# Optimization experiments

Measured on AMD Instinct MI355X. Metric: run time of the kernel, lower is better.

The kernel has to match this reference:

```python
import jax, jax.numpy as jnp
import numpy as np

N_NODES = 50000
DEG = 16
N_EDGES = N_NODES * DEG
IN_FEATS = 256
NUM_HEADS = 4
OUT_FEATS = 64
NEG_SLOPE = 0.2


def setup_inputs() -> dict:
    key = jax.random.key(0)
    k1, k2, k3, k4, k5, k6 = jax.random.split(key, 6)
    row_ptr = jnp.arange(N_NODES + 1, dtype=jnp.int64 if jax.config.jax_enable_x64 else jnp.int32) * DEG
    col_ind = jax.random.randint(k1, (N_EDGES,), 0, N_NODES)
    # CSC mirrors (used only by the fused op's backward pass; math-inert here)
    col_ptr = jnp.arange(N_NODES + 1, dtype=row_ptr.dtype) * DEG
    row_ind = jax.random.randint(k2, (N_EDGES,), 0, N_NODES)
    feat = jax.random.normal(k3, (N_NODES, IN_FEATS), dtype=jnp.float32)
    # Glorot-style init for params
    g = float(np.sqrt(2.0))  # gain for relu
    std_W = g * np.sqrt(2.0 / (IN_FEATS + OUT_FEATS * NUM_HEADS))
    W = jax.random.normal(k4, (IN_FEATS, OUT_FEATS * NUM_HEADS), dtype=jnp.float32) * std_W
    std_a = g * np.sqrt(2.0 / (1 + NUM_HEADS * OUT_FEATS))
    attn_l = jax.random.normal(k5, (1, NUM_HEADS, OUT_FEATS), dtype=jnp.float32) * std_a
    attn_r = jax.random.normal(k6, (1, NUM_HEADS, OUT_FEATS), dtype=jnp.float32) * std_a
    return {"row_ptr": row_ptr, "col_ind": col_ind, "col_ptr": col_ptr,
            "row_ind": row_ind, "feat": feat, "W": W, "attn_l": attn_l, "attn_r": attn_r}


def reference(row_ptr, col_ind, col_ptr, row_ind, feat, W, attn_l, attn_r):
    N = feat.shape[0]
    E = col_ind.shape[0]
    # Dense projection: [N, H, F]
    h = jnp.matmul(feat, W).reshape(N, NUM_HEADS, OUT_FEATS)
    attn_row = jnp.sum(attn_l * h, axis=-1)  # [N, H] (dst scores)
    attn_col = jnp.sum(attn_r * h, axis=-1)  # [N, H] (src scores)
    # Recover destination node id per edge from CSR row_ptr
    dst = jnp.searchsorted(row_ptr, jnp.arange(E), side="right") - 1  # [E]
    src = col_ind  # [E]
    # Edge score: LeakyReLU(attn_row[dst] + attn_col[src])
    e = attn_row[dst] + attn_col[src]  # [E, H]
    e = jnp.where(e > 0, e, NEG_SLOPE * e)
    # Segment softmax over each destination's neighborhood
    e_max = jax.ops.segment_max(e, dst, num_segments=N)  # [N, H]
    ex = jnp.exp(e - e_max[dst])  # [E, H]
    denom = jax.ops.segment_sum(ex, dst, num_segments=N)  # [N, H]
    alpha = ex / denom[dst]  # [E, H]
    # Weighted scatter-add aggregation of source features
    out = jax.ops.segment_sum(h[src] * alpha[:, :, None], dst, num_segments=N)  # [N, H, F]
    return out
```

## Files before the change

kernel.cpp:

```cpp
#include <hip/hip_runtime.h>
#include <hip/hip_bf16.h>

#define DEG        16
#define IN_FEATS   256
#define NUM_HEADS  4
#define OUT_FEATS  64
#define HF         256
#define NEG_SLOPE  0.2f

#define CPITCH 264

typedef __attribute__((ext_vector_type(8))) short  short8;
typedef __attribute__((ext_vector_type(4))) float  floatx4;
typedef unsigned short ushortT;

__device__ __forceinline__ unsigned short f2bf(float f) {
    union { float f; unsigned u; } v; v.f = f;
    unsigned r = v.u + 0x7fffu + ((v.u >> 16) & 1u);
    return (unsigned short)(r >> 16);
}
__device__ __forceinline__ float bf_lo(unsigned u) {
    union { unsigned x; float f; } v; v.x = u << 16; return v.f;
}
__device__ __forceinline__ float bf_hi(unsigned u) {
    union { unsigned x; float f; } v; v.x = u & 0xffff0000u; return v.f;
}
__device__ __forceinline__ unsigned cvt2(float lo, float hi) {
    return (unsigned)f2bf(lo) | ((unsigned)f2bf(hi) << 16);
}

__global__ __launch_bounds__(256) void conv_wt(
    const float* __restrict__ W, ushortT* __restrict__ Wt)
{
    int n = blockIdx.x;
    int k = threadIdx.x;
    Wt[n * 256 + k] = f2bf(W[k * 256 + n]);
}

__global__ __launch_bounds__(256) void gat_gemm_fused(
    const float* __restrict__ feat,
    const ushortT* __restrict__ Bt,
    const float* __restrict__ attn_l,
    const float* __restrict__ attn_r,
    ushortT* __restrict__ Hb,
    float* __restrict__ arow,
    float* __restrict__ acol,
    int M)
{
    __shared__ __align__(16) ushortT SMEM[32 * CPITCH];
    ushortT* As = SMEM;
    ushortT* Cs = SMEM;

    const int tid  = threadIdx.x;
    const int wave = tid >> 6;
    const int lane = tid & 63;
    const int l15  = lane & 15;
    const int quad = lane >> 4;
    const int rowBase = blockIdx.x * 32;

    short8 bbuf[2][4];
    #pragma unroll
    for (int ni = 0; ni < 4; ++ni)
        bbuf[0][ni] = *(const short8*)&Bt[(wave * 64 + ni * 16 + l15) * 256 + quad * 8];

    {
        float4 v[8];
        #pragma unroll
        for (int i = 0; i < 8; ++i) {
            int id  = i * 256 + tid;
            int row = id >> 6;
            int c4  = id & 63;
            int gr  = rowBase + row; if (gr > M - 1) gr = M - 1;
            v[i] = *(const float4*)&feat[(size_t)gr * 256 + c4 * 4];
        }
        #pragma unroll
        for (int i = 0; i < 8; ++i) {
            int id   = i * 256 + tid;
            int row  = id >> 6;
            int c4   = id & 63;
            int cg   = c4 >> 1;
            int half = c4 & 1;
            uint2 w = make_uint2(cvt2(v[i].x, v[i].y), cvt2(v[i].z, v[i].w));
            *(uint2*)&As[row * 256 + ((cg ^ (row & 7)) << 3) + half * 4] = w;
        }
    }

    __syncthreads();

    floatx4 acc[2][4] = {};

    #pragma unroll
    for (int ks = 0; ks < 8; ++ks) {
        if (ks < 7) {
            #pragma unroll
            for (int ni = 0; ni < 4; ++ni)
                bbuf[(ks + 1) & 1][ni] = *(const short8*)
                    &Bt[(wave * 64 + ni * 16 + l15) * 256 + (ks + 1) * 32 + quad * 8];
        }
        short8 af[2];
        #pragma unroll
        for (int mi = 0; mi < 2; ++mi) {
            int row = mi * 16 + l15;
            int q   = ks * 4 + quad;
            int cst = q ^ (row & 7);
            af[mi] = *(const short8*)&As[row * 256 + cst * 8];
        }
        #pragma unroll
        for (int mi = 0; mi < 2; ++mi)
            #pragma unroll
            for (int ni = 0; ni < 4; ++ni)
                acc[mi][ni] = __builtin_amdgcn_mfma_f32_16x16x32_bf16(
                    af[mi], bbuf[ks & 1][ni], acc[mi][ni], 0, 0, 0);
    }

    float al[4], ar[4];
    #pragma unroll
    for (int ni = 0; ni < 4; ++ni) {
        al[ni] = attn_l[wave * 64 + ni * 16 + l15];
        ar[ni] = attn_r[wave * 64 + ni * 16 + l15];
    }
    #pragma unroll
    for (int mi = 0; mi < 2; ++mi) {
        #pragma unroll
        for (int reg = 0; reg < 4; ++reg) {
            float pl = 0.f, pr = 0.f;
            #pragma unroll
            for (int ni = 0; ni < 4; ++ni) {
                pl = fmaf(acc[mi][ni][reg], al[ni], pl);
                pr = fmaf(acc[mi][ni][reg], ar[ni], pr);
            }
            #pragma unroll
            for (int off = 8; off >= 1; off >>= 1) {
                pl += __shfl_xor(pl, off, 64);
                pr += __shfl_xor(pr, off, 64);
            }
            if (l15 == 0) {
                int gr = rowBase + mi * 16 + quad * 4 + reg;
                if (gr < M) {
                    arow[gr * NUM_HEADS + wave] = pl;
                    acol[gr * NUM_HEADS + wave] = pr;
                }
            }
        }
    }

    __syncthreads();

    #pragma unroll
    for (int mi = 0; mi < 2; ++mi)
        #pragma unroll
        for (int ni = 0; ni < 4; ++ni)
            #pragma unroll
            for (int reg = 0; reg < 4; ++reg)
                Cs[(mi * 16 + quad * 4 + reg) * CPITCH + wave * 64 + ni * 16 + l15] =
                    f2bf(acc[mi][ni][reg]);
    __syncthreads();

    #pragma unroll
    for (int i = 0; i < 4; ++i) {
        int f  = tid + 256 * i;
        int r  = f >> 5;
        int c8 = (f & 31) << 3;
        int gr = rowBase + r;
        if (gr < M) {
            uint4 v = *(const uint4*)&Cs[r * CPITCH + c8];
            *(uint4*)&Hb[(size_t)gr * HF + c8] = v;
        }
    }
}

__global__ __launch_bounds__(256) void gat_aggregate9(
    const ushortT* __restrict__ Hb,
    const float* __restrict__ arow,
    const float* __restrict__ acol,
    const int* __restrict__ col_ind,
    float* __restrict__ out,
    int N)
{
    const int tid  = threadIdx.x;
    const int wave = tid >> 6;
    const int lane = tid & 63;
    const int gw   = blockIdx.x * 4 + wave;

    int nA = gw * 2;
    if (nA >= N) return;
    int nB = nA + 1;
    const bool hasB = (nB < N);
    if (!hasB) nB = nA;

    const int j16  = lane & 15;
    const int hd16 = lane >> 4;

    int srcA = col_ind[nA * DEG + j16];
    int srcB = col_ind[nB * DEG + j16];
    float eA = arow[nA * NUM_HEADS + hd16] + acol[srcA * NUM_HEADS + hd16];
    float eB = arow[nB * NUM_HEADS + hd16] + acol[srcB * NUM_HEADS + hd16];
    eA = (eA > 0.f) ? eA : NEG_SLOPE * eA;
    eB = (eB > 0.f) ? eB : NEG_SLOPE * eB;

    float mA = eA, mB = eB;
    #pragma unroll
    for (int off = 8; off >= 1; off >>= 1) {
        mA = fmaxf(mA, __shfl_xor(mA, off, 16));
        mB = fmaxf(mB, __shfl_xor(mB, off, 16));
    }
    float exA = __expf(eA - mA), exB = __expf(eB - mB);
    float sA = exA, sB = exB;
    #pragma unroll
    for (int off = 8; off >= 1; off >>= 1) {
        sA += __shfl_xor(sA, off, 16);
        sB += __shfl_xor(sB, off, 16);
    }
    float alA = exA / sA;
    float alB = exB / sB;

    const int l32     = lane & 31;
    const int half    = lane >> 5;
    const int headSel = (l32 >> 3) << 4;

    int   sjA[8], sjB[8];
    float avA[8], avB[8];
    #pragma unroll
    for (int j = 0; j < 8; ++j) {
        int ep = (j << 1) + half;
        sjA[j] = __shfl(srcA, ep, 64);
        avA[j] = __shfl(alA, headSel + ep, 64);
        sjB[j] = __shfl(srcB, ep, 64);
        avB[j] = __shfl(alB, headSel + ep, 64);
    }

    uint4 vA[8], vB[8];
    #pragma unroll
    for (int j = 0; j < 8; ++j)
        vA[j] = *(const uint4*)&Hb[(size_t)sjA[j] * HF + l32 * 8];
    #pragma unroll
    for (int j = 0; j < 8; ++j)
        vB[j] = *(const uint4*)&Hb[(size_t)sjB[j] * HF + l32 * 8];

    __builtin_amdgcn_sched_barrier(0);

    float accA[8] = {}, accB[8] = {};
    #pragma unroll
    for (int j = 0; j < 8; ++j) {
        accA[0] = fmaf(avA[j], bf_lo(vA[j].x), accA[0]);
        accA[1] = fmaf(avA[j], bf_hi(vA[j].x), accA[1]);
        accA[2] = fmaf(avA[j], bf_lo(vA[j].y), accA[2]);
        accA[3] = fmaf(avA[j], bf_hi(vA[j].y), accA[3]);
        accA[4] = fmaf(avA[j], bf_lo(vA[j].z), accA[4]);
        accA[5] = fmaf(avA[j], bf_hi(vA[j].z), accA[5]);
        accA[6] = fmaf(avA[j], bf_lo(vA[j].w), accA[6]);
        accA[7] = fmaf(avA[j], bf_hi(vA[j].w), accA[7]);
    }
    #pragma unroll
    for (int j = 0; j < 8; ++j) {
        accB[0] = fmaf(avB[j], bf_lo(vB[j].x), accB[0]);
        accB[1] = fmaf(avB[j], bf_hi(vB[j].x), accB[1]);
        accB[2] = fmaf(avB[j], bf_lo(vB[j].y), accB[2]);
        accB[3] = fmaf(avB[j], bf_hi(vB[j].y), accB[3]);
        accB[4] = fmaf(avB[j], bf_lo(vB[j].z), accB[4]);
        accB[5] = fmaf(avB[j], bf_hi(vB[j].z), accB[5]);
        accB[6] = fmaf(avB[j], bf_lo(vB[j].w), accB[6]);
        accB[7] = fmaf(avB[j], bf_hi(vB[j].w), accB[7]);
    }

    #pragma unroll
    for (int i = 0; i < 8; ++i) {
        accA[i] += __shfl_xor(accA[i], 32, 64);
        accB[i] += __shfl_xor(accB[i], 32, 64);
    }

    float4 oA, oB;
    if (half == 0) {
        oA = make_float4(accA[0], accA[1], accA[2], accA[3]);
        oB = make_float4(accB[0], accB[1], accB[2], accB[3]);
    } else {
        oA = make_float4(accA[4], accA[5], accA[6], accA[7]);
        oB = make_float4(accB[4], accB[5], accB[6], accB[7]);
    }
    *(float4*)&out[(size_t)nA * HF + l32 * 8 + half * 4] = oA;
    if (hasB)
        *(float4*)&out[(size_t)nB * HF + l32 * 8 + half * 4] = oB;
}

extern "C" void kernel_launch(void* const* d_in, const int* in_sizes, int n_in,
                              void* d_out, int out_size, void* d_ws, size_t ws_size,
                              hipStream_t stream) {
    const int*   col_ind = (const int*)  d_in[1];
    const float* feat    = (const float*)d_in[4];
    const float* W       = (const float*)d_in[5];
    const float* attn_l  = (const float*)d_in[6];
    const float* attn_r  = (const float*)d_in[7];
    float* out = (float*)d_out;

    const int N = in_sizes[0] - 1;

    ushortT* Hb   = (ushortT*)d_ws;
    float*   arow = (float*)(Hb + (size_t)N * HF);
    float*   acol = arow + (size_t)N * NUM_HEADS;
    ushortT* Wt   = (ushortT*)(acol + (size_t)N * NUM_HEADS);

    conv_wt<<<256, 256, 0, stream>>>(W, Wt);

    dim3 ggrid((N + 31) / 32);
    gat_gemm_fused<<<ggrid, 256, 0, stream>>>(feat, Wt, attn_l, attn_r,
                                              Hb, arow, acol, N);

    gat_aggregate9<<<(N + 7) / 8, 256, 0, stream>>>(Hb, arow, acol, col_ind, out, N);
}
```

Baseline: 195.6 us.

## Make GEMM kernel persistent with register-resident W and prefetched feature tiles

Converts the projection GEMM into a persistent kernel with 512 blocks that loop over 32-row tiles. Each wave loads its whole bf16 W slice into registers once instead of streaming it per tile. The next tile's feature rows are prefetched into registers while the current tile runs its MFMAs. This cuts repeated W traffic and per-block launch and setup cost, but the 32 short8 register arrays raise VGPR pressure, which may lower occupancy or cause spills.

```diff
diff --git a/kernel.cpp b/kernel.cpp
--- a/kernel.cpp
+++ b/kernel.cpp
@@ -45,7 +45,7 @@
     ushortT* __restrict__ Hb,
     float* __restrict__ arow,
     float* __restrict__ acol,
-    int M)
+    int M, int nTiles)
 {
     __shared__ __align__(16) ushortT SMEM[32 * CPITCH];
     ushortT* As = SMEM;
@@ -56,23 +56,38 @@
     const int lane = tid & 63;
     const int l15  = lane & 15;
     const int quad = lane >> 4;
-    const int rowBase = blockIdx.x * 32;
-
-    short8 bbuf[2][4];
-    #pragma unroll
-    for (int ni = 0; ni < 4; ++ni)
-        bbuf[0][ni] = *(const short8*)&Bt[(wave * 64 + ni * 16 + l15) * 256 + quad * 8];
-
-    {
-        float4 v[8];
+
+    short8 Breg[8][4];
+    #pragma unroll
+    for (int ks = 0; ks < 8; ++ks)
+        #pragma unroll
+        for (int ni = 0; ni < 4; ++ni)
+            Breg[ks][ni] = *(const short8*)
+                &Bt[(wave * 64 + ni * 16 + l15) * 256 + ks * 32 + quad * 8];
+
+    float al[4], ar[4];
+    #pragma unroll
+    for (int ni = 0; ni < 4; ++ni) {
+        al[ni] = attn_l[wave * 64 + ni * 16 + l15];
+        ar[ni] = attn_r[wave * 64 + ni * 16 + l15];
+    }
+
+    int t = blockIdx.x;
+    float4 v[8];
+    if (t < nTiles) {
         #pragma unroll
         for (int i = 0; i < 8; ++i) {
             int id  = i * 256 + tid;
             int row = id >> 6;
             int c4  = id & 63;
-            int gr  = rowBase + row; if (gr > M - 1) gr = M - 1;
+            int gr  = t * 32 + row; if (gr > M - 1) gr = M - 1;
             v[i] = *(const float4*)&feat[(size_t)gr * 256 + c4 * 4];
         }
+    }
+
+    for (; t < nTiles; t += gridDim.x) {
+        const int rowBase = t * 32;
+
         #pragma unroll
         for (int i = 0; i < 8; ++i) {
             int id   = i * 256 + tid;
@@ -83,89 +98,90 @@
             uint2 w = make_uint2(cvt2(v[i].x, v[i].y), cvt2(v[i].z, v[i].w));
             *(uint2*)&As[row * 256 + ((cg ^ (row & 7)) << 3) + half * 4] = w;
         }
-    }
-
-    __syncthreads();
-
-    floatx4 acc[2][4] = {};
-
-    #pragma unroll
-    for (int ks = 0; ks < 8; ++ks) {
-        if (ks < 7) {
+        __syncthreads();
+
+        {
+            int t2 = t + gridDim.x;
+            if (t2 < nTiles) {
+                #pragma unroll
+                for (int i = 0; i < 8; ++i) {
+                    int id  = i * 256 + tid;
+                    int row = id >> 6;
+                    int c4  = id & 63;
+                    int gr  = t2 * 32 + row; if (gr > M - 1) gr = M - 1;
+                    v[i] = *(const float4*)&feat[(size_t)gr * 256 + c4 * 4];
+                }
+            }
+        }
+
+        floatx4 acc[2][4] = {};
+        #pragma unroll
+        for (int ks = 0; ks < 8; ++ks) {
+            short8 af[2];
             #pragma unroll
-            for (int ni = 0; ni < 4; ++ni)
-                bbuf[(ks + 1) & 1][ni] = *(const short8*)
-                    &Bt[(wave * 64 + ni * 16 + l15) * 256 + (ks + 1) * 32 + quad * 8];
-        }
-        short8 af[2];
+            for (int mi = 0; mi < 2; ++mi) {
+                int row = mi * 16 + l15;
+                int q   = ks * 4 + quad;
+                int cst = q ^ (row & 7);
+                af[mi] = *(const short8*)&As[row * 256 + cst * 8];
+            }
+            #pragma unroll
+            for (int mi = 0; mi < 2; ++mi)
+                #pragma unroll
+                for (int ni = 0; ni < 4; ++ni)
+                    acc[mi][ni] = __builtin_amdgcn_mfma_f32_16x16x32_bf16(
+                        af[mi], Breg[ks][ni], acc[mi][ni], 0, 0, 0);
+        }
+
         #pragma unroll
         for (int mi = 0; mi < 2; ++mi) {
-            int row = mi * 16 + l15;
-            int q   = ks * 4 + quad;
-            int cst = q ^ (row & 7);
-            af[mi] = *(const short8*)&As[row * 256 + cst * 8];
-        }
+            #pragma unroll
+            for (int reg = 0; reg < 4; ++reg) {
+                float pl = 0.f, pr = 0.f;
+                #pragma unroll
+                for (int ni = 0; ni < 4; ++ni) {
+                    pl = fmaf(acc[mi][ni][reg], al[ni], pl);
+                    pr = fmaf(acc[mi][ni][reg], ar[ni], pr);
+                }
+                #pragma unroll
+                for (int off = 8; off >= 1; off >>= 1) {
+                    pl += __shfl_xor(pl, off, 64);
+                    pr += __shfl_xor(pr, off, 64);
+                }
+                if (l15 == 0) {
+                    int gr = rowBase + mi * 16 + quad * 4 + reg;
+                    if (gr < M) {
+                        arow[gr * NUM_HEADS + wave] = pl;
+                        acol[gr * NUM_HEADS + wave] = pr;
+                    }
+                }
+            }
+        }
+
+        __syncthreads();
+
         #pragma unroll
         for (int mi = 0; mi < 2; ++mi)
             #pragma unroll
             for (int ni = 0; ni < 4; ++ni)
-                acc[mi][ni] = __builtin_amdgcn_mfma_f32_16x16x32_bf16(
-                    af[mi], bbuf[ks & 1][ni], acc[mi][ni], 0, 0, 0);
-    }
-
-    float al[4], ar[4];
-    #pragma unroll
-    for (int ni = 0; ni < 4; ++ni) {
-        al[ni] = attn_l[wave * 64 + ni * 16 + l15];
-        ar[ni] = attn_r[wave * 64 + ni * 16 + l15];
-    }
-    #pragma unroll
-    for (int mi = 0; mi < 2; ++mi) {
-        #pragma unroll
-        for (int reg = 0; reg < 4; ++reg) {
-            float pl = 0.f, pr = 0.f;
-            #pragma unroll
-            for (int ni = 0; ni < 4; ++ni) {
-                pl = fmaf(acc[mi][ni][reg], al[ni], pl);
-                pr = fmaf(acc[mi][ni][reg], ar[ni], pr);
+                #pragma unroll
+                for (int reg = 0; reg < 4; ++reg)
+                    Cs[(mi * 16 + quad * 4 + reg) * CPITCH + wave * 64 + ni * 16 + l15] =
+                        f2bf(acc[mi][ni][reg]);
+        __syncthreads();
+
+        #pragma unroll
+        for (int i = 0; i < 4; ++i) {
+            int f  = tid + 256 * i;
+            int r  = f >> 5;
+            int c8 = (f & 31) << 3;
+            int gr = rowBase + r;
+            if (gr < M) {
+                uint4 w = *(const uint4*)&Cs[r * CPITCH + c8];
+                *(uint4*)&Hb[(size_t)gr * HF + c8] = w;
             }
-            #pragma unroll
-            for (int off = 8; off >= 1; off >>= 1) {
-                pl += __shfl_xor(pl, off, 64);
-                pr += __shfl_xor(pr, off, 64);
-            }
-            if (l15 == 0) {
-                int gr = rowBase + mi * 16 + quad * 4 + reg;
-                if (gr < M) {
-                    arow[gr * NUM_HEADS + wave] = pl;
-                    acol[gr * NUM_HEADS + wave] = pr;
-                }
-            }
-        }
-    }
-
-    __syncthreads();
-
-    #pragma unroll
-    for (int mi = 0; mi < 2; ++mi)
-        #pragma unroll
-        for (int ni = 0; ni < 4; ++ni)
-            #pragma unroll
-            for (int reg = 0; reg < 4; ++reg)
-                Cs[(mi * 16 + quad * 4 + reg) * CPITCH + wave * 64 + ni * 16 + l15] =
-                    f2bf(acc[mi][ni][reg]);
-    __syncthreads();
-
-    #pragma unroll
-    for (int i = 0; i < 4; ++i) {
-        int f  = tid + 256 * i;
-        int r  = f >> 5;
-        int c8 = (f & 31) << 3;
-        int gr = rowBase + r;
-        if (gr < M) {
-            uint4 v = *(const uint4*)&Cs[r * CPITCH + c8];
-            *(uint4*)&Hb[(size_t)gr * HF + c8] = v;
-        }
+        }
+        __syncthreads();
     }
 }
 
@@ -301,9 +317,11 @@
 
     conv_wt<<<256, 256, 0, stream>>>(W, Wt);
 
-    dim3 ggrid((N + 31) / 32);
-    gat_gemm_fused<<<ggrid, 256, 0, stream>>>(feat, Wt, attn_l, attn_r,
-                                              Hb, arow, acol, N);
+    int nTiles = (N + 31) / 32;
+    int gblocks = 512;
+    if (gblocks > nTiles) gblocks = nTiles;
+    gat_gemm_fused<<<gblocks, 256, 0, stream>>>(feat, Wt, attn_l, attn_r,
+                                                Hb, arow, acol, N, nTiles);
 
     gat_aggregate9<<<(N + 7) / 8, 256, 0, stream>>>(Hb, arow, acol, col_ind, out, N);
 }
```

Result: no change. 197.7 us (+1.1%).
